# Kernel optimization log

Measured on AMD Instinct MI355X. Metric: run time of the kernel, lower is better.

Reference implementation:

```python
import jax, jax.numpy as jnp
import numpy as np

TEMPERATURE = 0.07
EPS = 1e-8          # torch cosine_similarity norm clamp
DIAG_FILL = 9e-15   # value masked_fill'ed onto the diagonal BEFORE temperature scaling


def setup_inputs() -> dict:
    key = jax.random.key(0)
    N, D = 16384, 128
    feats = jax.random.normal(key, (N, D), dtype=jnp.float32)
    # unique labels: required for the original torch code's broadcast
    # (-cos_sim[pos_mask] must have exactly N elements)
    labels = jnp.arange(N, dtype=jnp.int32).reshape(N, 1)
    return {"feats": feats, "labels": labels}


def reference(feats, labels):
    # cosine similarity matrix: normalize rows once, then a single GEMM
    norm = jnp.maximum(jnp.linalg.norm(feats, axis=-1, keepdims=True), EPS)
    f = feats / norm
    cos_sim = f @ f.T                                   # [N, N]

    N = cos_sim.shape[0]
    eye = jnp.eye(N, dtype=bool)
    cos_sim = jnp.where(eye, DIAG_FILL, cos_sim)        # masked_fill_(self_mask, 9e-15)
    cos_sim = cos_sim / TEMPERATURE

    pos_mask = labels == labels.T                       # [N, N] bool, one True per row
    # cos_sim[pos_mask] with exactly one positive per row == masked row-sum
    pos = jnp.sum(jnp.where(pos_mask, cos_sim, 0.0), axis=-1)  # [N]

    nll = -pos + jax.nn.logsumexp(cos_sim, axis=-1)     # [N]
    return jnp.mean(nll)
```

## Files before the change

### kernel.cpp

```cpp
#include <hip/hip_runtime.h>
#include <hip/hip_bf16.h>
#include <stdint.h>

typedef __attribute__((ext_vector_type(8))) short short8;
typedef __attribute__((ext_vector_type(4))) float f32x4;

#define N_ROWS 16384
#define DIM 128

constexpr float ALPHA = 4.5398160f;
constexpr float POSC = 1.2857143e-13f;

__device__ __forceinline__ void gload_lds16(const void* g, void* lds) {
  __builtin_amdgcn_global_load_lds(
      (const __attribute__((address_space(1))) void*)(uintptr_t)g,
      (__attribute__((address_space(3))) void*)(uintptr_t)lds,
      16, 0, 0);
}

__global__ void normalize_kernel(const float* __restrict__ feats,
                                 unsigned short* __restrict__ G,
                                 float* __restrict__ rowsum) {
  const int tid  = threadIdx.x;
  const int lane = tid & 63;
  const int row  = blockIdx.x * 4 + (tid >> 6);

  const float2 v = *(const float2*)(feats + (size_t)row * DIM + lane * 2);
  float ss = v.x * v.x + v.y * v.y;
#pragma unroll
  for (int m = 1; m < 64; m <<= 1) ss += __shfl_xor(ss, m);
  const float sc = ALPHA / fmaxf(sqrtf(ss), 1e-8f);

  __hip_bfloat16 h0 = __float2bfloat16(v.x * sc);
  __hip_bfloat16 h1 = __float2bfloat16(v.y * sc);
  unsigned int packed = (unsigned int)(*(unsigned short*)&h0) |
                        ((unsigned int)(*(unsigned short*)&h1) << 16);
  *(unsigned int*)(G + (size_t)row * DIM + lane * 2) = packed;

  if (blockIdx.x < 64) rowsum[blockIdx.x * 256 + tid] = 0.f;
}

__global__ __launch_bounds__(256, 2) void simclr_lse_kernel(
    const unsigned short* __restrict__ G, float* __restrict__ rowsum) {
  const int tid  = threadIdx.x;
  const int lane = tid & 63;
  const int w    = tid >> 6;
  const int wr   = w >> 1;
  const int wc   = w & 1;
  const int c    = lane & 15;
  const int q    = lane >> 4;

  const int p   = blockIdx.x >> 4;
  const int s   = blockIdx.x & 15;
  const int r16 = p & 15;
  const int jb = (s * 129 + r16) >> 4;
  const int je = ((s + 1) * 129 + r16) >> 4;
  const int split = 128 - p;

  __shared__ __align__(16) unsigned short Tbuf[128 * 128];

  unsigned goff[8];
#pragma unroll
  for (int t = 0; t < 8; ++t) {
    const int cidx = t * 256 + tid;
    const int col  = cidx >> 4;
    const int kc   = (cidx & 15) ^ (col & 15);
    goff[t] = (unsigned)(col * DIM + kc * 8);
  }

  unsigned boff[4][4];
#pragma unroll
  for (int tc = 0; tc < 4; ++tc)
#pragma unroll
    for (int ks = 0; ks < 4; ++ks) {
      const int col = wc * 64 + tc * 16 + c;
      const int kc  = ks * 4 + q;
      boff[tc][ks] = (unsigned)((col * 16 + (kc ^ c)) * 16);
    }

  const f32x4 zero4 = {0.f, 0.f, 0.f, 0.f};
  const short* Gs = (const short*)G;

  for (int sg = 0; sg < 2; ++sg) {
    int rt, cbeg, nct;
    if (sg == 0) {
      rt   = p;
      cbeg = p + jb;
      nct  = min(je, split) - jb;
    } else {
      rt   = 127 - p;
      const int t0 = max(jb, split);
      cbeg = t0 - 1;
      nct  = je - t0;
    }
    if (nct <= 0) continue;

    const int rbw = rt * 128 + wr * 64;

    short8 afrag[4][4];
#pragma unroll
    for (int tr = 0; tr < 4; ++tr)
#pragma unroll
      for (int ks = 0; ks < 4; ++ks) {
        const int row = rbw + tr * 16 + c;
        afrag[tr][ks] = *(const short8*)(Gs + (size_t)row * DIM + ks * 32 + q * 8);
      }

    float rs[4][4];
#pragma unroll
    for (int tr = 0; tr < 4; ++tr)
#pragma unroll
      for (int r = 0; r < 4; ++r) rs[tr][r] = 0.f;

    for (int jj = 0; jj < nct; ++jj) {
      const int ct = cbeg + jj;
      __syncthreads();
      {
        const unsigned short* gsrc = G + (size_t)ct * 128 * DIM;
#pragma unroll
        for (int t = 0; t < 8; ++t)
          gload_lds16(gsrc + goff[t],
                      (void*)(Tbuf + (size_t)(t * 256 + w * 64) * 8));
      }
      __syncthreads();

      f32x4 acc[4][4];
#pragma unroll
      for (int ks = 0; ks < 4; ++ks) {
        short8 bfr[4];
#pragma unroll
        for (int tc = 0; tc < 4; ++tc)
          bfr[tc] = *(const short8*)((const char*)Tbuf + boff[tc][ks]);
#pragma unroll
        for (int tr = 0; tr < 4; ++tr)
#pragma unroll
          for (int tc = 0; tc < 4; ++tc) {
            if (ks == 0)
              acc[tr][tc] = __builtin_amdgcn_mfma_f32_16x16x32_bf16(
                  afrag[tr][0], bfr[tc], zero4, 0, 0, 0);
            else
              acc[tr][tc] = __builtin_amdgcn_mfma_f32_16x16x32_bf16(
                  afrag[tr][ks], bfr[tc], acc[tr][tc], 0, 0, 0);
          }
      }

      if (ct == rt && wr == wc) {
#pragma unroll
        for (int tr = 0; tr < 4; ++tr)
#pragma unroll
          for (int r = 0; r < 4; ++r)
            if (c == q * 4 + r) acc[tr][tr][r] = 0.f;
      }

      const bool mirror = (ct != rt);
      float cs[4] = {0.f, 0.f, 0.f, 0.f};
#pragma unroll
      for (int tr = 0; tr < 4; ++tr)
#pragma unroll
        for (int tc = 0; tc < 4; ++tc) {
          const float e0 = __builtin_amdgcn_exp2f(acc[tr][tc][0]);
          const float e1 = __builtin_amdgcn_exp2f(acc[tr][tc][1]);
          const float e2 = __builtin_amdgcn_exp2f(acc[tr][tc][2]);
          const float e3 = __builtin_amdgcn_exp2f(acc[tr][tc][3]);
          rs[tr][0] += e0;
          rs[tr][1] += e1;
          rs[tr][2] += e2;
          rs[tr][3] += e3;
          if (mirror) cs[tc] += (e0 + e1) + (e2 + e3);
        }

      if (mirror) {
#pragma unroll
        for (int tc = 0; tc < 4; ++tc) {
          float v = cs[tc];
          v += __shfl_xor(v, 16);
          v += __shfl_xor(v, 32);
          if (q == 0)
            atomicAdd(&rowsum[ct * 128 + wc * 64 + tc * 16 + c], v);
        }
      }
    }

#pragma unroll
    for (int tr = 0; tr < 4; ++tr)
#pragma unroll
      for (int r = 0; r < 4; ++r) {
        float v = rs[tr][r];
        v += __shfl_xor(v, 1);
        v += __shfl_xor(v, 2);
        v += __shfl_xor(v, 4);
        v += __shfl_xor(v, 8);
        if (c == 0) atomicAdd(&rowsum[rbw + tr * 16 + q * 4 + r], v);
      }
  }
}

__global__ void finalize_kernel(const float* __restrict__ rowsum,
                                float* __restrict__ out) {
  const int tid = threadIdx.x;
  float local = 0.f;
  for (int i = tid; i < N_ROWS; i += 1024) local += logf(rowsum[i]);
#pragma unroll
  for (int m = 1; m < 64; m <<= 1) local += __shfl_xor(local, m);
  __shared__ float part[16];
  if ((tid & 63) == 0) part[tid >> 6] = local;
  __syncthreads();
  if (tid == 0) {
    float s = 0.f;
#pragma unroll
    for (int i = 0; i < 16; ++i) s += part[i];
    out[0] = s / (float)N_ROWS - POSC;
  }
}

extern "C" void kernel_launch(void* const* d_in, const int* in_sizes, int n_in,
                              void* d_out, int out_size, void* d_ws, size_t ws_size,
                              hipStream_t stream) {
  (void)in_sizes; (void)n_in; (void)out_size; (void)ws_size;
  const float* feats = (const float*)d_in[0];
  unsigned short* G = (unsigned short*)d_ws;
  float* rowsum = (float*)((char*)d_ws + (size_t)N_ROWS * DIM * 2);

  normalize_kernel<<<dim3(N_ROWS / 4), dim3(256), 0, stream>>>(feats, G, rowsum);
  simclr_lse_kernel<<<dim3(1024), dim3(256), 0, stream>>>(G, rowsum);
  finalize_kernel<<<dim3(1), dim3(1024), 0, stream>>>(rowsum, d_out ? (float*)d_out : nullptr);
}
```

Baseline: 128.2 us.

## Double-buffer half column tiles and rebalance grid to 768 blocks

Splits each 128-column tile into two 64-column halves held in a double-buffered LDS ring, prefetching the next half while MFMAs run on the current one, which removes one barrier per step. LDS per block stays at 32KB, launch bounds rise to 3 blocks per SM, and the grid shrinks to 768 blocks (12 segments per row pair) to match the CUs. The narrower B tile lowers the MFMA-to-load ratio per A fragment and adds more atomics per processed column.

```diff
diff --git a/kernel.cpp b/kernel.cpp
--- a/kernel.cpp
+++ b/kernel.cpp
@@ -40,7 +40,7 @@
   if (blockIdx.x < 64) rowsum[blockIdx.x * 256 + tid] = 0.f;
 }
 
-__global__ __launch_bounds__(256, 2) void simclr_lse_kernel(
+__global__ __launch_bounds__(256, 3) void simclr_lse_kernel(
     const unsigned short* __restrict__ G, float* __restrict__ rowsum) {
   const int tid  = threadIdx.x;
   const int lane = tid & 63;
@@ -50,32 +50,32 @@
   const int c    = lane & 15;
   const int q    = lane >> 4;
 
-  const int p   = blockIdx.x >> 4;
-  const int s   = blockIdx.x & 15;
-  const int r16 = p & 15;
-  const int jb = (s * 129 + r16) >> 4;
-  const int je = ((s + 1) * 129 + r16) >> 4;
+  const int p   = blockIdx.x / 12;
+  const int s   = blockIdx.x % 12;
+  const int rot = p % 12;
+  const int jb = (s * 129 + rot) / 12;
+  const int je = ((s + 1) * 129 + rot) / 12;
   const int split = 128 - p;
 
-  __shared__ __align__(16) unsigned short Tbuf[128 * 128];
-
-  unsigned goff[8];
-#pragma unroll
-  for (int t = 0; t < 8; ++t) {
+  __shared__ __align__(16) unsigned short Tbuf[2][64 * 128];
+
+  unsigned goff[4];
+#pragma unroll
+  for (int t = 0; t < 4; ++t) {
     const int cidx = t * 256 + tid;
     const int col  = cidx >> 4;
     const int kc   = (cidx & 15) ^ (col & 15);
     goff[t] = (unsigned)(col * DIM + kc * 8);
   }
 
-  unsigned boff[4][4];
-#pragma unroll
-  for (int tc = 0; tc < 4; ++tc)
+  unsigned boff[2][4];
+#pragma unroll
+  for (int tc = 0; tc < 2; ++tc)
 #pragma unroll
     for (int ks = 0; ks < 4; ++ks) {
-      const int col = wc * 64 + tc * 16 + c;
-      const int kc  = ks * 4 + q;
-      boff[tc][ks] = (unsigned)((col * 16 + (kc ^ c)) * 16);
+      const int line = wc * 32 + tc * 16 + c;
+      const int kc   = ks * 4 + q;
+      boff[tc][ks] = (unsigned)((line * 16 + (kc ^ c)) * 16);
     }
 
   const f32x4 zero4 = {0.f, 0.f, 0.f, 0.f};
@@ -112,29 +112,44 @@
 #pragma unroll
       for (int r = 0; r < 4; ++r) rs[tr][r] = 0.f;
 
-    for (int jj = 0; jj < nct; ++jj) {
-      const int ct = cbeg + jj;
+    __syncthreads();
+    {
+      const unsigned short* gsrc = G + (size_t)(cbeg * 128) * DIM;
+#pragma unroll
+      for (int t = 0; t < 4; ++t)
+        gload_lds16(gsrc + goff[t],
+                    (void*)(&Tbuf[0][0] + (size_t)(t * 256 + w * 64) * 8));
+    }
+
+    const int total = nct * 2;
+    for (int m = 0; m < total; ++m) {
+      const int ct  = cbeg + (m >> 1);
+      const int h   = m & 1;
+      const int buf = m & 1;
       __syncthreads();
-      {
-        const unsigned short* gsrc = G + (size_t)ct * 128 * DIM;
-#pragma unroll
-        for (int t = 0; t < 8; ++t)
+
+      if (m + 1 < total) {
+        const int m2 = m + 1;
+        const unsigned short* gsrc =
+            G + (size_t)((cbeg + (m2 >> 1)) * 128 + (m2 & 1) * 64) * DIM;
+#pragma unroll
+        for (int t = 0; t < 4; ++t)
           gload_lds16(gsrc + goff[t],
-                      (void*)(Tbuf + (size_t)(t * 256 + w * 64) * 8));
-      }
-      __syncthreads();
-
-      f32x4 acc[4][4];
+                      (void*)(&Tbuf[m2 & 1][0] + (size_t)(t * 256 + w * 64) * 8));
+      }
+
+      const char* bbase = (const char*)&Tbuf[buf][0];
+      f32x4 acc[4][2];
 #pragma unroll
       for (int ks = 0; ks < 4; ++ks) {
-        short8 bfr[4];
-#pragma unroll
-        for (int tc = 0; tc < 4; ++tc)
-          bfr[tc] = *(const short8*)((const char*)Tbuf + boff[tc][ks]);
+        short8 bfr[2];
+#pragma unroll
+        for (int tc = 0; tc < 2; ++tc)
+          bfr[tc] = *(const short8*)(bbase + boff[tc][ks]);
 #pragma unroll
         for (int tr = 0; tr < 4; ++tr)
 #pragma unroll
-          for (int tc = 0; tc < 4; ++tc) {
+          for (int tc = 0; tc < 2; ++tc) {
             if (ks == 0)
               acc[tr][tc] = __builtin_amdgcn_mfma_f32_16x16x32_bf16(
                   afrag[tr][0], bfr[tc], zero4, 0, 0, 0);
@@ -144,20 +159,22 @@
           }
       }
 
-      if (ct == rt && wr == wc) {
-#pragma unroll
-        for (int tr = 0; tr < 4; ++tr)
+      if (ct == rt && h == wr) {
+#pragma unroll
+        for (int tc = 0; tc < 2; ++tc) {
+          const int tr = wc * 2 + tc;
 #pragma unroll
           for (int r = 0; r < 4; ++r)
-            if (c == q * 4 + r) acc[tr][tr][r] = 0.f;
+            if (c == q * 4 + r) acc[tr][tc][r] = 0.f;
+        }
       }
 
       const bool mirror = (ct != rt);
-      float cs[4] = {0.f, 0.f, 0.f, 0.f};
+      float cs[2] = {0.f, 0.f};
 #pragma unroll
       for (int tr = 0; tr < 4; ++tr)
 #pragma unroll
-        for (int tc = 0; tc < 4; ++tc) {
+        for (int tc = 0; tc < 2; ++tc) {
           const float e0 = __builtin_amdgcn_exp2f(acc[tr][tc][0]);
           const float e1 = __builtin_amdgcn_exp2f(acc[tr][tc][1]);
           const float e2 = __builtin_amdgcn_exp2f(acc[tr][tc][2]);
@@ -171,12 +188,12 @@
 
       if (mirror) {
 #pragma unroll
-        for (int tc = 0; tc < 4; ++tc) {
+        for (int tc = 0; tc < 2; ++tc) {
           float v = cs[tc];
           v += __shfl_xor(v, 16);
           v += __shfl_xor(v, 32);
           if (q == 0)
-            atomicAdd(&rowsum[ct * 128 + wc * 64 + tc * 16 + c], v);
+            atomicAdd(&rowsum[ct * 128 + h * 64 + wc * 32 + tc * 16 + c], v);
         }
       }
     }
@@ -222,6 +239,6 @@
   float* rowsum = (float*)((char*)d_ws + (size_t)N_ROWS * DIM * 2);
 
   normalize_kernel<<<dim3(N_ROWS / 4), dim3(256), 0, stream>>>(feats, G, rowsum);
-  simclr_lse_kernel<<<dim3(1024), dim3(256), 0, stream>>>(G, rowsum);
+  simclr_lse_kernel<<<dim3(768), dim3(256), 0, stream>>>(G, rowsum);
   finalize_kernel<<<dim3(1), dim3(1024), 0, stream>>>(rowsum, d_out ? (float*)d_out : nullptr);
 }
```

New measurement: 184.7 us. 1.44x slower.
